# Optimization experiments

Hardware: AMD Instinct MI355X
Metric: run time of the kernel (lower is better)

The kernel has to match this reference:

```python
import jax, jax.numpy as jnp
import numpy as np

D = 2048
H = 16
DH = D // H  # 128
THETA = 10000.0

def _rope(x, pos):
    # x: (..., S, DH); pos: (S,) absolute positions
    freqs = 1.0 / THETA ** (jnp.arange(0, DH, 2, dtype=jnp.float32) / DH)  # (DH/2,)
    emb = pos[:, None].astype(jnp.float32) * freqs[None, :]                # (S, DH/2)
    cos = jnp.concatenate([jnp.cos(emb), jnp.cos(emb)], axis=-1)          # tile like torch .repeat(...,2)
    sin = jnp.concatenate([jnp.sin(emb), jnp.sin(emb)], axis=-1)
    x1, x2 = x[..., : DH // 2], x[..., DH // 2 :]
    rot = jnp.concatenate([-x2, x1], axis=-1)  # rotate_half
    return x * cos + rot * sin

def setup_inputs() -> dict:
    key = jax.random.key(0)
    ks = jax.random.split(key, 4)
    B, S = 2, 2048
    return {
        "x": jax.random.normal(ks[0], (B, S, D), jnp.float32),
        "wq": 0.01 * jax.random.normal(ks[1], (D, D), jnp.float32),
        "wkv": 0.01 * jax.random.normal(ks[2], (D, 2 * DH), jnp.float32),
        "wo": 0.01 * jax.random.normal(ks[3], (D, D), jnp.float32),
        "past_length": 0,
    }

def reference(x, wq, wkv, wo, past_length):
    B, S, _ = x.shape
    Q = x @ wq.T                       # (B,S,D)
    KV = x @ wkv                       # (B,S,2*DH)
    K, V = KV[..., :DH], KV[..., DH:]  # single shared KV head (B,S,DH)
    # no kv_cache (prefill): S_full = past_length + S with past_length=0
    S_full = past_length + S
    q = Q.reshape(B, S, H, DH).transpose(0, 2, 1, 3)   # (B,H,S,DH)
    q = _rope(q, past_length + jnp.arange(S))
    k = _rope(K, jnp.arange(S_full))                    # (B,S_full,DH), unreplicated
    scores = jnp.einsum('bhsd,btd->bhst', q, k) / np.float32(np.sqrt(DH))
    i = jnp.arange(S)[:, None]
    j = jnp.arange(S_full)[None, :]
    causal = j <= i + past_length                       # tril(diagonal=past_length)
    scores = jnp.where(causal[None, None], scores, -jnp.inf)
    attn = jax.nn.softmax(scores, axis=-1)
    o = jnp.einsum('bhst,btd->bhsd', attn, V)           # (B,H,S,DH)
    o = o.transpose(0, 2, 1, 3).reshape(B, S, D)
    out = o @ wo.T
    return (out, K, V)  # output + updated kv cache
```

## Files before the change

kernel.cpp:

```cpp
#include <hip/hip_runtime.h>
#include <hip/hip_bf16.h>
#include <cstdint>


typedef __attribute__((ext_vector_type(8))) __bf16 bf16x8;
typedef __attribute__((ext_vector_type(4))) float f32x4;
typedef __attribute__((ext_vector_type(16))) float f32x16;
typedef __attribute__((ext_vector_type(4))) float floatv4;
typedef __attribute__((ext_vector_type(4))) unsigned short ushortv4;
typedef __attribute__((ext_vector_type(4))) unsigned int uintv4;

#define LOG2E 1.4426950408889634f

__device__ __forceinline__ unsigned short f2bf(float f) {
    union { float f; unsigned u; } v; v.f = f;
    unsigned r = v.u + 0x7fffu + ((v.u >> 16) & 1u);
    return (unsigned short)(r >> 16);
}

__device__ __forceinline__ unsigned pk2(float a, float b) {
    return (unsigned)f2bf(a) | ((unsigned)f2bf(b) << 16);
}

__device__ __forceinline__ f32x16 zero16() {
    f32x16 z;
#pragma unroll
    for (int i = 0; i < 16; ++i) z[i] = 0.f;
    return z;
}

#define GLL16(g, l)                                                                   \
    __builtin_amdgcn_global_load_lds(                                                 \
        (const __attribute__((address_space(1))) void*)(uintptr_t)(g),                \
        (__attribute__((address_space(3))) void*)(unsigned)(uintptr_t)(l), 16, 0, 0)

__global__ __launch_bounds__(256) void cast_bf16_k(const float* __restrict__ src,
                                                   unsigned short* __restrict__ dst, int n4) {
    int i = blockIdx.x * 256 + threadIdx.x;
    if (i >= n4) return;
    floatv4 v = reinterpret_cast<const floatv4*>(src)[i];
    ushortv4 o;
    o.x = f2bf(v.x); o.y = f2bf(v.y); o.z = f2bf(v.z); o.w = f2bf(v.w);
    reinterpret_cast<ushortv4*>(dst)[i] = o;
}

__global__ __launch_bounds__(256) void cast_t_wkv_k(const float* __restrict__ src,
                                                    unsigned short* __restrict__ dst) {
    int i = blockIdx.x * 256 + threadIdx.x;
    int k = i >> 8, j = i & 255;
    dst[j * 2048 + k] = f2bf(src[i]);
}

__global__ __launch_bounds__(256) void gemm_bt(const unsigned short* __restrict__ A,
                                               const unsigned short* __restrict__ B,
                                               float* __restrict__ C,
                                               int M, int N, int K) {
    __shared__ __align__(16) unsigned short As[4096];
    __shared__ __align__(16) unsigned short Bs[4096];
    const int tid  = threadIdx.x;
    const int lane = tid & 63;
    const int wid  = tid >> 6;
    const int wr   = wid >> 1;
    const int wc   = wid & 1;
    const size_t row0 = (size_t)blockIdx.y * 128;
    const size_t col0 = (size_t)blockIdx.x * 128;
    f32x4 acc[4][4];
#pragma unroll
    for (int m = 0; m < 4; ++m)
#pragma unroll
        for (int n = 0; n < 4; ++n) acc[m][n] = (f32x4){0.f, 0.f, 0.f, 0.f};

    const int srow = tid >> 2;
    const int scol = (tid & 3) << 3;
    const unsigned short* Ag = A + (row0 + srow) * (size_t)K + scol;
    const unsigned short* Bg = B + (col0 + srow) * (size_t)K + scol;
    unsigned short* AsW = &As[wid << 9];
    unsigned short* BsW = &Bs[wid << 9];

    const int lrow = lane & 15;
    const int lk   = (lane >> 4) << 3;

    for (int k0 = 0; k0 < K; k0 += 32) {
        GLL16(Ag + k0, AsW);
        GLL16(Ag + k0 + (size_t)64 * K, AsW + 2048);
        GLL16(Bg + k0, BsW);
        GLL16(Bg + k0 + (size_t)64 * K, BsW + 2048);
        __syncthreads();
        bf16x8 af[4], bfr[4];
#pragma unroll
        for (int m = 0; m < 4; ++m)
            af[m] = *reinterpret_cast<const bf16x8*>(&As[(wr * 64 + m * 16 + lrow) * 32 + lk]);
#pragma unroll
        for (int n = 0; n < 4; ++n)
            bfr[n] = *reinterpret_cast<const bf16x8*>(&Bs[(wc * 64 + n * 16 + lrow) * 32 + lk]);
#pragma unroll
        for (int m = 0; m < 4; ++m)
#pragma unroll
            for (int n = 0; n < 4; ++n)
                acc[m][n] = __builtin_amdgcn_mfma_f32_16x16x32_bf16(af[m], bfr[n], acc[m][n], 0, 0, 0);
        __syncthreads();
    }
    const size_t orow0 = row0 + wr * 64 + ((lane >> 4) << 2);
    const size_t ocol  = col0 + wc * 64 + lrow;
#pragma unroll
    for (int m = 0; m < 4; ++m)
#pragma unroll
        for (int n = 0; n < 4; ++n)
#pragma unroll
            for (int r = 0; r < 4; ++r)
                C[(orow0 + m * 16 + r) * (size_t)N + ocol + n * 16] = acc[m][n][r];
}

__global__ __launch_bounds__(256) void rope_pack_k(const float* __restrict__ Qf,
                                                   const float* __restrict__ KVf,
                                                   unsigned short* __restrict__ Qb,
                                                   unsigned short* __restrict__ Kb,
                                                   unsigned short* __restrict__ Vt,
                                                   float* __restrict__ Kout,
                                                   float* __restrict__ Vout) {
    const int row = blockIdx.x;
    const int b = row >> 11;
    const int s = row & 2047;
    const int t = threadIdx.x;
    const float* qrow = Qf + (size_t)row * 2048;
#pragma unroll
    for (int it = 0; it < 4; ++it) {
        int p = t + it * 256;
        int h = p >> 6;
        int i = p & 63;
        float fr  = exp2f(-(float)i * 0.20762050593045858f);
        float ang = (float)s * fr;
        float sn, c;
        sincosf(ang, &sn, &c);
        float x1 = qrow[h * 128 + i];
        float x2 = qrow[h * 128 + i + 64];
        size_t qb = (((size_t)(b * 16 + h)) * 2048 + s) * 128;
        Qb[qb + i]      = f2bf(x1 * c - x2 * sn);
        Qb[qb + i + 64] = f2bf(x2 * c + x1 * sn);
    }
    const float* kvrow = KVf + (size_t)row * 256;
    if (t < 128) {
        float kv = kvrow[t];
        float vv = kvrow[128 + t];
        Kout[(size_t)row * 128 + t] = kv;
        Vout[(size_t)row * 128 + t] = vv;
        Vt[((size_t)(b * 128 + t)) * 2048 + s] = f2bf(vv);
    }
    if (t < 64) {
        float fr  = exp2f(-(float)t * 0.20762050593045858f);
        float ang = (float)s * fr;
        float sn, c;
        sincosf(ang, &sn, &c);
        float x1 = kvrow[t];
        float x2 = kvrow[t + 64];
        size_t ko = ((size_t)b * 2048 + s) * 128;
        Kb[ko + t]      = f2bf(x1 * c - x2 * sn);
        Kb[ko + t + 64] = f2bf(x2 * c + x1 * sn);
    }
}

__global__ __launch_bounds__(256, 2) void attn_k(const unsigned short* __restrict__ Qb,
                                                 const unsigned short* __restrict__ Kb,
                                                 const unsigned short* __restrict__ Vt,
                                                 unsigned short* __restrict__ Ob) {
    const int h = blockIdx.y, b = blockIdx.z;
    const int lane = threadIdx.x & 63;
    const int w = threadIdx.x >> 6;
    const int tb = blockIdx.x * 4 + w;
    const int t = b ? (63 - tb) : tb;
    const int q0 = t * 32;
    const int lq = lane & 31;
    const int hl = lane >> 5;
    const int kofs = hl * 8;

    const unsigned short* qp = Qb + (((size_t)(b * 16 + h)) * 2048 + q0 + lq) * 128 + kofs;
    bf16x8 qf[8];
#pragma unroll
    for (int c = 0; c < 8; ++c)
        qf[c] = *reinterpret_cast<const bf16x8*>(qp + 16 * c);

    f32x16 O[4];
#pragma unroll
    for (int dt = 0; dt < 4; ++dt) O[dt] = zero16();
    float m = -1e30f, l = 0.f;

    const int nkt = t / 2 + 1;
    const unsigned short* kb = Kb + (size_t)b * 2048 * 128;
    const unsigned short* vb = Vt + (size_t)b * 128 * 2048;
    const float csc = 0.12751782377892224f;

    for (int kt = 0; kt < nkt; ++kt) {
        f32x16 S0 = zero16(), S1 = zero16();
        const unsigned short* kp0 = kb + ((size_t)(64 * kt + lq)) * 128 + kofs;
        const unsigned short* kp1 = kp0 + 32 * 128;
#pragma unroll
        for (int c = 0; c < 8; ++c) {
            bf16x8 k0 = *reinterpret_cast<const bf16x8*>(kp0 + 16 * c);
            bf16x8 k1 = *reinterpret_cast<const bf16x8*>(kp1 + 16 * c);
            S0 = __builtin_amdgcn_mfma_f32_32x32x16_bf16(k0, qf[c], S0, 0, 0, 0);
            S1 = __builtin_amdgcn_mfma_f32_32x32x16_bf16(k1, qf[c], S1, 0, 0, 0);
        }
        float sc[32];
        const bool lastt = (kt == nkt - 1);
#pragma unroll
        for (int s = 0; s < 2; ++s)
#pragma unroll
            for (int r = 0; r < 16; ++r) {
                float v = (s ? S1[r] : S0[r]) * csc;
                if (lastt) {
                    int key = 64 * kt + 32 * s + (r & 3) + 8 * (r >> 2) + 4 * hl;
                    if (key > q0 + lq) v = -3.0e38f;
                }
                sc[16 * s + r] = v;
            }
        float tm[16];
#pragma unroll
        for (int i = 0; i < 16; ++i) tm[i] = fmaxf(sc[i], sc[i + 16]);
#pragma unroll
        for (int st = 8; st > 0; st >>= 1)
#pragma unroll
            for (int i = 0; i < st; ++i) tm[i] = fmaxf(tm[i], tm[i + st]);
        float mt = fmaxf(tm[0], __shfl_xor(tm[0], 32));
        float mn = fmaxf(m, mt);
        float corr = __builtin_amdgcn_exp2f(m - mn);
        m = mn;
#pragma unroll
        for (int i = 0; i < 32; ++i) sc[i] = __builtin_amdgcn_exp2f(sc[i] - mn);
        float ts[16];
#pragma unroll
        for (int i = 0; i < 16; ++i) ts[i] = sc[i] + sc[i + 16];
#pragma unroll
        for (int st = 8; st > 0; st >>= 1)
#pragma unroll
            for (int i = 0; i < st; ++i) ts[i] += ts[i + st];
        float sum = ts[0] + __shfl_xor(ts[0], 32);
        l = l * corr + sum;
#pragma unroll
        for (int dt = 0; dt < 4; ++dt)
#pragma unroll
            for (int r = 0; r < 16; ++r) O[dt][r] *= corr;
        unsigned pw[4][4];
#pragma unroll
        for (int s = 0; s < 2; ++s)
#pragma unroll
            for (int c2 = 0; c2 < 2; ++c2) {
                const int rb = 16 * s + 8 * c2;
                unsigned X0 = pk2(sc[rb + 0], sc[rb + 1]);
                unsigned X1 = pk2(sc[rb + 2], sc[rb + 3]);
                unsigned X2 = pk2(sc[rb + 4], sc[rb + 5]);
                unsigned X3 = pk2(sc[rb + 6], sc[rb + 7]);
                unsigned y0 = __shfl_xor(X0, 32);
                unsigned y1 = __shfl_xor(X1, 32);
                unsigned y2 = __shfl_xor(X2, 32);
                unsigned y3 = __shfl_xor(X3, 32);
                const int kc = 2 * s + c2;
                pw[kc][0] = hl ? y2 : X0;
                pw[kc][1] = hl ? y3 : X1;
                pw[kc][2] = hl ? X2 : y0;
                pw[kc][3] = hl ? X3 : y1;
            }
#pragma unroll
        for (int kc = 0; kc < 4; ++kc) {
            uintv4 u;
            u.x = pw[kc][0]; u.y = pw[kc][1]; u.z = pw[kc][2]; u.w = pw[kc][3];
            bf16x8 pf = __builtin_bit_cast(bf16x8, u);
            const unsigned short* vp = vb + (size_t)lq * 2048 + 64 * kt + 16 * kc + kofs;
#pragma unroll
            for (int dt = 0; dt < 4; ++dt) {
                bf16x8 vf = *reinterpret_cast<const bf16x8*>(vp + (size_t)(32 * dt) * 2048);
                O[dt] = __builtin_amdgcn_mfma_f32_32x32x16_bf16(vf, pf, O[dt], 0, 0, 0);
            }
        }
    }
    float invl = 1.f / l;
    unsigned short* ob = Ob + ((size_t)(b * 2048 + q0 + lq)) * 2048 + h * 128;
#pragma unroll
    for (int dt = 0; dt < 4; ++dt)
#pragma unroll
        for (int g = 0; g < 4; ++g) {
            ushortv4 ov;
            ov.x = f2bf(O[dt][4 * g + 0] * invl);
            ov.y = f2bf(O[dt][4 * g + 1] * invl);
            ov.z = f2bf(O[dt][4 * g + 2] * invl);
            ov.w = f2bf(O[dt][4 * g + 3] * invl);
            *reinterpret_cast<ushortv4*>(ob + 32 * dt + 8 * g + 4 * hl) = ov;
        }
}

extern "C" void kernel_launch(void* const* d_in, const int* in_sizes, int n_in,
                              void* d_out, int out_size, void* d_ws, size_t ws_size,
                              hipStream_t stream) {
    const float* x   = (const float*)d_in[0];
    const float* wq  = (const float*)d_in[1];
    const float* wkv = (const float*)d_in[2];
    const float* wo  = (const float*)d_in[3];

    float* out  = (float*)d_out;
    float* Kout = out + 8388608;
    float* Vout = Kout + 524288;

    char* ws = (char*)d_ws;
    unsigned short* xb   = (unsigned short*)(ws + 0);
    unsigned short* wqb  = (unsigned short*)(ws + 16777216);
    unsigned short* wkvT = (unsigned short*)(ws + 25165824);
    unsigned short* wob  = (unsigned short*)(ws + 26214400);
    float*          KVf  = (float*)(ws + 34603008);
    float*          Qf   = (float*)(ws + 38797312);
    unsigned short* Qb   = (unsigned short*)(ws + 0);
    unsigned short* Kb   = (unsigned short*)(ws + 16777216);
    unsigned short* Vt   = (unsigned short*)(ws + 17825792);
    unsigned short* Ob   = (unsigned short*)(ws + 34603008);

    cast_bf16_k<<<8192, 256, 0, stream>>>(x,  xb,  2097152);
    cast_bf16_k<<<4096, 256, 0, stream>>>(wq, wqb, 1048576);
    cast_bf16_k<<<4096, 256, 0, stream>>>(wo, wob, 1048576);
    cast_t_wkv_k<<<2048, 256, 0, stream>>>(wkv, wkvT);

    gemm_bt<<<dim3(2, 32),  256, 0, stream>>>(xb, wkvT, KVf, 4096, 256,  2048);
    gemm_bt<<<dim3(16, 32), 256, 0, stream>>>(xb, wqb,  Qf,  4096, 2048, 2048);

    rope_pack_k<<<4096, 256, 0, stream>>>(Qf, KVf, Qb, Kb, Vt, Kout, Vout);

    attn_k<<<dim3(16, 16, 2), 256, 0, stream>>>(Qb, Kb, Vt, Ob);

    gemm_bt<<<dim3(16, 32), 256, 0, stream>>>(Ob, wob, out, 4096, 2048, 2048);
}
```

Baseline: 480.0 us.

## Software-pipeline K/V loads with double-buffered registers in attention loop

The attention loop now prefetches the next key tile into a second register buffer while the current tile is processed. After the QK MFMAs it reuses the current K buffer to load the V tile ahead of the softmax. Loop iterations alternate between two buffers through a lambda so global-load latency can overlap the softmax math. This raises register pressure, which may lower occupancy or cause spills.

```diff
diff --git a/kernel.cpp b/kernel.cpp
--- a/kernel.cpp
+++ b/kernel.cpp
@@ -9,8 +9,6 @@
 typedef __attribute__((ext_vector_type(4))) float floatv4;
 typedef __attribute__((ext_vector_type(4))) unsigned short ushortv4;
 typedef __attribute__((ext_vector_type(4))) unsigned int uintv4;
-
-#define LOG2E 1.4426950408889634f
 
 __device__ __forceinline__ unsigned short f2bf(float f) {
     union { float f; unsigned u; } v; v.f = f;
@@ -189,16 +187,37 @@
     const unsigned short* vb = Vt + (size_t)b * 128 * 2048;
     const float csc = 0.12751782377892224f;
 
-    for (int kt = 0; kt < nkt; ++kt) {
+    bf16x8 bufA[16], bufB[16];
+    {
+        const unsigned short* kp = kb + (size_t)lq * 128 + kofs;
+#pragma unroll
+        for (int c = 0; c < 8; ++c) {
+            bufA[c]     = *reinterpret_cast<const bf16x8*>(kp + 16 * c);
+            bufA[8 + c] = *reinterpret_cast<const bf16x8*>(kp + 32 * 128 + 16 * c);
+        }
+    }
+
+    int kt = 0;
+    auto STEP = [&](bf16x8 (&Kc)[16], bf16x8 (&Kn)[16]) {
         f32x16 S0 = zero16(), S1 = zero16();
-        const unsigned short* kp0 = kb + ((size_t)(64 * kt + lq)) * 128 + kofs;
-        const unsigned short* kp1 = kp0 + 32 * 128;
 #pragma unroll
         for (int c = 0; c < 8; ++c) {
-            bf16x8 k0 = *reinterpret_cast<const bf16x8*>(kp0 + 16 * c);
-            bf16x8 k1 = *reinterpret_cast<const bf16x8*>(kp1 + 16 * c);
-            S0 = __builtin_amdgcn_mfma_f32_32x32x16_bf16(k0, qf[c], S0, 0, 0, 0);
-            S1 = __builtin_amdgcn_mfma_f32_32x32x16_bf16(k1, qf[c], S1, 0, 0, 0);
+            S0 = __builtin_amdgcn_mfma_f32_32x32x16_bf16(Kc[c],     qf[c], S0, 0, 0, 0);
+            S1 = __builtin_amdgcn_mfma_f32_32x32x16_bf16(Kc[8 + c], qf[c], S1, 0, 0, 0);
+        }
+        const unsigned short* vp = vb + (size_t)lq * 2048 + 64 * kt + kofs;
+#pragma unroll
+        for (int dt = 0; dt < 4; ++dt)
+#pragma unroll
+            for (int kc = 0; kc < 4; ++kc)
+                Kc[4 * dt + kc] =
+                    *reinterpret_cast<const bf16x8*>(vp + (size_t)(32 * dt) * 2048 + 16 * kc);
+        const int ktn = (kt + 1 < nkt) ? (kt + 1) : kt;
+        const unsigned short* kp = kb + (size_t)(64 * ktn + lq) * 128 + kofs;
+#pragma unroll
+        for (int c = 0; c < 8; ++c) {
+            Kn[c]     = *reinterpret_cast<const bf16x8*>(kp + 16 * c);
+            Kn[8 + c] = *reinterpret_cast<const bf16x8*>(kp + 32 * 128 + 16 * c);
         }
         float sc[32];
         const bool lastt = (kt == nkt - 1);
@@ -233,8 +252,7 @@
         for (int st = 8; st > 0; st >>= 1)
 #pragma unroll
             for (int i = 0; i < st; ++i) ts[i] += ts[i + st];
-        float sum = ts[0] + __shfl_xor(ts[0], 32);
-        l = l * corr + sum;
+        l = l * corr + ts[0] + __shfl_xor(ts[0], 32);
 #pragma unroll
         for (int dt = 0; dt < 4; ++dt)
 #pragma unroll
@@ -264,14 +282,19 @@
             uintv4 u;
             u.x = pw[kc][0]; u.y = pw[kc][1]; u.z = pw[kc][2]; u.w = pw[kc][3];
             bf16x8 pf = __builtin_bit_cast(bf16x8, u);
-            const unsigned short* vp = vb + (size_t)lq * 2048 + 64 * kt + 16 * kc + kofs;
-#pragma unroll
-            for (int dt = 0; dt < 4; ++dt) {
-                bf16x8 vf = *reinterpret_cast<const bf16x8*>(vp + (size_t)(32 * dt) * 2048);
-                O[dt] = __builtin_amdgcn_mfma_f32_32x32x16_bf16(vf, pf, O[dt], 0, 0, 0);
-            }
-        }
-    }
+#pragma unroll
+            for (int dt = 0; dt < 4; ++dt)
+                O[dt] = __builtin_amdgcn_mfma_f32_32x32x16_bf16(Kc[4 * dt + kc], pf, O[dt], 0, 0, 0);
+        }
+    };
+
+    for (;;) {
+        STEP(bufA, bufB);
+        if (++kt == nkt) break;
+        STEP(bufB, bufA);
+        if (++kt == nkt) break;
+    }
+
     float invl = 1.f / l;
     unsigned short* ob = Ob + ((size_t)(b * 2048 + q0 + lq)) * 2048 + h * 128;
 #pragma unroll
```

Result: faster. 433.5 us (-9.7%).

## Stage K/V tiles in swizzled shared memory shared across block waves

Applied to the files above, without the earlier changes.

The attention kernel now stages each 64-key K tile and V^T tile into XOR-swizzled LDS using a GLL16 global-to-LDS load macro. All four waves then read their MFMA operands from LDS instead of each loading from global memory separately. Blocks are also reordered to run the longest causal work first (g = 15 - blockIdx.x), replacing the per-batch reversal. This adds two __syncthreads per tile with no double buffering, and waves with shorter causal extents sit idle at the barriers.

```diff
diff --git a/kernel.cpp b/kernel.cpp
--- a/kernel.cpp
+++ b/kernel.cpp
@@ -9,8 +9,6 @@
 typedef __attribute__((ext_vector_type(4))) float floatv4;
 typedef __attribute__((ext_vector_type(4))) unsigned short ushortv4;
 typedef __attribute__((ext_vector_type(4))) unsigned int uintv4;
-
-#define LOG2E 1.4426950408889634f
 
 __device__ __forceinline__ unsigned short f2bf(float f) {
     union { float f; unsigned u; } v; v.f = f;
@@ -163,15 +161,37 @@
                                                  const unsigned short* __restrict__ Kb,
                                                  const unsigned short* __restrict__ Vt,
                                                  unsigned short* __restrict__ Ob) {
+    const int g = 15 - blockIdx.x;
     const int h = blockIdx.y, b = blockIdx.z;
     const int lane = threadIdx.x & 63;
     const int w = threadIdx.x >> 6;
-    const int tb = blockIdx.x * 4 + w;
-    const int t = b ? (63 - tb) : tb;
-    const int q0 = t * 32;
+    const int j = 4 * g + w;
+    const int q0 = j * 32;
     const int lq = lane & 31;
     const int hl = lane >> 5;
     const int kofs = hl * 8;
+    const int my_nkt = 2 * g + 1 + (w >> 1);
+    const int NKT = 2 * g + 2;
+
+    __shared__ __align__(16) unsigned short Ks[8192];
+    __shared__ __align__(16) unsigned short Vs[8192];
+
+    const unsigned short* kbB = Kb + (size_t)b * 2048 * 128;
+    const unsigned short* vtB = Vt + (size_t)b * 128 * 2048;
+    const float csc = 0.12751782377892224f;
+
+    int k_r[4], k_gc[4], v_d[4], v_kg[4];
+    unsigned short *kdst[4], *vdst[4];
+#pragma unroll
+    for (int c = 0; c < 4; ++c) {
+        int G = w * 256 + c * 64 + lane;
+        int r = G >> 4;
+        int gc = (G & 15) ^ (r & 15);
+        k_r[c] = r; k_gc[c] = gc;
+        v_d[c] = r * 2 + (gc >> 3); v_kg[c] = gc & 7;
+        kdst[c] = Ks + (w * 2048 + c * 512);
+        vdst[c] = Vs + (w * 2048 + c * 512);
+    }
 
     const unsigned short* qp = Qb + (((size_t)(b * 16 + h)) * 2048 + q0 + lq) * 128 + kofs;
     bf16x8 qf[8];
@@ -184,106 +204,119 @@
     for (int dt = 0; dt < 4; ++dt) O[dt] = zero16();
     float m = -1e30f, l = 0.f;
 
-    const int nkt = t / 2 + 1;
-    const unsigned short* kb = Kb + (size_t)b * 2048 * 128;
-    const unsigned short* vb = Vt + (size_t)b * 128 * 2048;
-    const float csc = 0.12751782377892224f;
-
-    for (int kt = 0; kt < nkt; ++kt) {
-        f32x16 S0 = zero16(), S1 = zero16();
-        const unsigned short* kp0 = kb + ((size_t)(64 * kt + lq)) * 128 + kofs;
-        const unsigned short* kp1 = kp0 + 32 * 128;
-#pragma unroll
-        for (int c = 0; c < 8; ++c) {
-            bf16x8 k0 = *reinterpret_cast<const bf16x8*>(kp0 + 16 * c);
-            bf16x8 k1 = *reinterpret_cast<const bf16x8*>(kp1 + 16 * c);
-            S0 = __builtin_amdgcn_mfma_f32_32x32x16_bf16(k0, qf[c], S0, 0, 0, 0);
-            S1 = __builtin_amdgcn_mfma_f32_32x32x16_bf16(k1, qf[c], S1, 0, 0, 0);
+    for (int kt = 0; kt < NKT; ++kt) {
+#pragma unroll
+        for (int c = 0; c < 4; ++c) {
+            GLL16(kbB + (size_t)(64 * kt + k_r[c]) * 128 + k_gc[c] * 8, kdst[c]);
+            GLL16(vtB + (size_t)v_d[c] * 2048 + kt * 64 + v_kg[c] * 8, vdst[c]);
         }
-        float sc[32];
-        const bool lastt = (kt == nkt - 1);
-#pragma unroll
-        for (int s = 0; s < 2; ++s)
-#pragma unroll
-            for (int r = 0; r < 16; ++r) {
-                float v = (s ? S1[r] : S0[r]) * csc;
-                if (lastt) {
-                    int key = 64 * kt + 32 * s + (r & 3) + 8 * (r >> 2) + 4 * hl;
-                    if (key > q0 + lq) v = -3.0e38f;
+        __syncthreads();
+        if (kt < my_nkt) {
+            bf16x8 kf0[8], kf1[8];
+            const int r0 = lq, r1 = lq + 32;
+#pragma unroll
+            for (int c = 0; c < 8; ++c) {
+                kf0[c] = *reinterpret_cast<const bf16x8*>(
+                    (const char*)Ks + r0 * 256 + (((2 * c + hl) ^ (r0 & 15)) * 16));
+                kf1[c] = *reinterpret_cast<const bf16x8*>(
+                    (const char*)Ks + r1 * 256 + (((2 * c + hl) ^ (r1 & 15)) * 16));
+            }
+            f32x16 S0 = zero16(), S1 = zero16();
+#pragma unroll
+            for (int c = 0; c < 8; ++c) {
+                S0 = __builtin_amdgcn_mfma_f32_32x32x16_bf16(kf0[c], qf[c], S0, 0, 0, 0);
+                S1 = __builtin_amdgcn_mfma_f32_32x32x16_bf16(kf1[c], qf[c], S1, 0, 0, 0);
+            }
+            float sc[32];
+            const bool lastt = (kt == my_nkt - 1);
+#pragma unroll
+            for (int s = 0; s < 2; ++s)
+#pragma unroll
+                for (int r = 0; r < 16; ++r) {
+                    float v = (s ? S1[r] : S0[r]) * csc;
+                    if (lastt) {
+                        int key = 64 * kt + 32 * s + (r & 3) + 8 * (r >> 2) + 4 * hl;
+                        if (key > q0 + lq) v = -3.0e38f;
+                    }
+                    sc[16 * s + r] = v;
                 }
-                sc[16 * s + r] = v;
-            }
-        float tm[16];
-#pragma unroll
-        for (int i = 0; i < 16; ++i) tm[i] = fmaxf(sc[i], sc[i + 16]);
-#pragma unroll
-        for (int st = 8; st > 0; st >>= 1)
-#pragma unroll
-            for (int i = 0; i < st; ++i) tm[i] = fmaxf(tm[i], tm[i + st]);
-        float mt = fmaxf(tm[0], __shfl_xor(tm[0], 32));
-        float mn = fmaxf(m, mt);
-        float corr = __builtin_amdgcn_exp2f(m - mn);
-        m = mn;
-#pragma unroll
-        for (int i = 0; i < 32; ++i) sc[i] = __builtin_amdgcn_exp2f(sc[i] - mn);
-        float ts[16];
-#pragma unroll
-        for (int i = 0; i < 16; ++i) ts[i] = sc[i] + sc[i + 16];
-#pragma unroll
-        for (int st = 8; st > 0; st >>= 1)
-#pragma unroll
-            for (int i = 0; i < st; ++i) ts[i] += ts[i + st];
-        float sum = ts[0] + __shfl_xor(ts[0], 32);
-        l = l * corr + sum;
-#pragma unroll
-        for (int dt = 0; dt < 4; ++dt)
-#pragma unroll
-            for (int r = 0; r < 16; ++r) O[dt][r] *= corr;
-        unsigned pw[4][4];
-#pragma unroll
-        for (int s = 0; s < 2; ++s)
-#pragma unroll
-            for (int c2 = 0; c2 < 2; ++c2) {
-                const int rb = 16 * s + 8 * c2;
-                unsigned X0 = pk2(sc[rb + 0], sc[rb + 1]);
-                unsigned X1 = pk2(sc[rb + 2], sc[rb + 3]);
-                unsigned X2 = pk2(sc[rb + 4], sc[rb + 5]);
-                unsigned X3 = pk2(sc[rb + 6], sc[rb + 7]);
-                unsigned y0 = __shfl_xor(X0, 32);
-                unsigned y1 = __shfl_xor(X1, 32);
-                unsigned y2 = __shfl_xor(X2, 32);
-                unsigned y3 = __shfl_xor(X3, 32);
-                const int kc = 2 * s + c2;
-                pw[kc][0] = hl ? y2 : X0;
-                pw[kc][1] = hl ? y3 : X1;
-                pw[kc][2] = hl ? X2 : y0;
-                pw[kc][3] = hl ? X3 : y1;
-            }
-#pragma unroll
-        for (int kc = 0; kc < 4; ++kc) {
-            uintv4 u;
-            u.x = pw[kc][0]; u.y = pw[kc][1]; u.z = pw[kc][2]; u.w = pw[kc][3];
-            bf16x8 pf = __builtin_bit_cast(bf16x8, u);
-            const unsigned short* vp = vb + (size_t)lq * 2048 + 64 * kt + 16 * kc + kofs;
-#pragma unroll
-            for (int dt = 0; dt < 4; ++dt) {
-                bf16x8 vf = *reinterpret_cast<const bf16x8*>(vp + (size_t)(32 * dt) * 2048);
-                O[dt] = __builtin_amdgcn_mfma_f32_32x32x16_bf16(vf, pf, O[dt], 0, 0, 0);
+            float tm[16];
+#pragma unroll
+            for (int i = 0; i < 16; ++i) tm[i] = fmaxf(sc[i], sc[i + 16]);
+#pragma unroll
+            for (int st = 8; st > 0; st >>= 1)
+#pragma unroll
+                for (int i = 0; i < st; ++i) tm[i] = fmaxf(tm[i], tm[i + st]);
+            float mt = fmaxf(tm[0], __shfl_xor(tm[0], 32));
+            float mn = fmaxf(m, mt);
+            float corr = __builtin_amdgcn_exp2f(m - mn);
+            m = mn;
+#pragma unroll
+            for (int i = 0; i < 32; ++i) sc[i] = __builtin_amdgcn_exp2f(sc[i] - mn);
+            float ts[16];
+#pragma unroll
+            for (int i = 0; i < 16; ++i) ts[i] = sc[i] + sc[i + 16];
+#pragma unroll
+            for (int st = 8; st > 0; st >>= 1)
+#pragma unroll
+                for (int i = 0; i < st; ++i) ts[i] += ts[i + st];
+            l = l * corr + ts[0] + __shfl_xor(ts[0], 32);
+#pragma unroll
+            for (int dt = 0; dt < 4; ++dt)
+#pragma unroll
+                for (int r = 0; r < 16; ++r) O[dt][r] *= corr;
+            unsigned pw[4][4];
+#pragma unroll
+            for (int s = 0; s < 2; ++s)
+#pragma unroll
+                for (int c2 = 0; c2 < 2; ++c2) {
+                    const int rb = 16 * s + 8 * c2;
+                    unsigned X0 = pk2(sc[rb + 0], sc[rb + 1]);
+                    unsigned X1 = pk2(sc[rb + 2], sc[rb + 3]);
+                    unsigned X2 = pk2(sc[rb + 4], sc[rb + 5]);
+                    unsigned X3 = pk2(sc[rb + 6], sc[rb + 7]);
+                    unsigned y0 = __shfl_xor(X0, 32);
+                    unsigned y1 = __shfl_xor(X1, 32);
+                    unsigned y2 = __shfl_xor(X2, 32);
+                    unsigned y3 = __shfl_xor(X3, 32);
+                    const int kc = 2 * s + c2;
+                    pw[kc][0] = hl ? y2 : X0;
+                    pw[kc][1] = hl ? y3 : X1;
+                    pw[kc][2] = hl ? X2 : y0;
+                    pw[kc][3] = hl ? X3 : y1;
+                }
+            const int vrow_lo = lq >> 1;
+            const int vpar8 = (lq & 1) * 8;
+#pragma unroll
+            for (int kc = 0; kc < 4; ++kc) {
+                uintv4 u;
+                u.x = pw[kc][0]; u.y = pw[kc][1]; u.z = pw[kc][2]; u.w = pw[kc][3];
+                bf16x8 pf = __builtin_bit_cast(bf16x8, u);
+                const int gcl = vpar8 + 2 * kc + hl;
+#pragma unroll
+                for (int dt = 0; dt < 4; ++dt) {
+                    const int vrow = 16 * dt + vrow_lo;
+                    bf16x8 vf = *reinterpret_cast<const bf16x8*>(
+                        (const char*)Vs + vrow * 256 + ((gcl ^ vrow_lo) * 16));
+                    O[dt] = __builtin_amdgcn_mfma_f32_32x32x16_bf16(vf, pf, O[dt], 0, 0, 0);
+                }
             }
         }
-    }
+        __syncthreads();
+    }
+
     float invl = 1.f / l;
     unsigned short* ob = Ob + ((size_t)(b * 2048 + q0 + lq)) * 2048 + h * 128;
 #pragma unroll
     for (int dt = 0; dt < 4; ++dt)
 #pragma unroll
-        for (int g = 0; g < 4; ++g) {
+        for (int gg = 0; gg < 4; ++gg) {
             ushortv4 ov;
-            ov.x = f2bf(O[dt][4 * g + 0] * invl);
-            ov.y = f2bf(O[dt][4 * g + 1] * invl);
-            ov.z = f2bf(O[dt][4 * g + 2] * invl);
-            ov.w = f2bf(O[dt][4 * g + 3] * invl);
-            *reinterpret_cast<ushortv4*>(ob + 32 * dt + 8 * g + 4 * hl) = ov;
+            ov.x = f2bf(O[dt][4 * gg + 0] * invl);
+            ov.y = f2bf(O[dt][4 * gg + 1] * invl);
+            ov.z = f2bf(O[dt][4 * gg + 2] * invl);
+            ov.w = f2bf(O[dt][4 * gg + 3] * invl);
+            *reinterpret_cast<ushortv4*>(ob + 32 * dt + 8 * gg + 4 * hl) = ov;
         }
 }
 
```

Result: faster. 386.6 us (-19.4%).
